# Performance work log

Measured on AMD Instinct MI355X. Metric: run time of the kernel, lower is better.

Reference implementation:

```python
import jax, jax.numpy as jnp
import numpy as np

# Farras first-stage analysis filters [tree][lp/hp][10 taps] (Selesnick fs_farras)
_FARRAS_AF = np.array([
    [[0.0, -0.08838834764832, 0.08838834764832, 0.69587998903400, 0.69587998903400, 0.08838834764832, -0.08838834764832, 0.01122679215254, 0.01122679215254, 0.0],
     [0.0, -0.01122679215254, 0.01122679215254, 0.08838834764832, 0.08838834764832, -0.69587998903400, 0.69587998903400, -0.08838834764832, -0.08838834764832, 0.0]],
    [[0.01122679215254, 0.01122679215254, -0.08838834764832, 0.08838834764832, 0.69587998903400, 0.69587998903400, 0.08838834764832, -0.08838834764832, 0.0, 0.0],
     [0.0, 0.0, -0.08838834764832, -0.08838834764832, 0.69587998903400, -0.69587998903400, 0.08838834764832, 0.08838834764832, 0.01122679215254, -0.01122679215254]]
], dtype=np.float32)

# Kingsbury Q-shift analysis filters (Selesnick dualfilt1)
_DUAL_AF = np.array([
    [[0.03516384, 0.0, -0.08832942, 0.23389032, 0.76027237, 0.58751830, 0.0, -0.11430184, 0.0, 0.0],
     [0.0, 0.0, -0.11430184, 0.0, 0.58751830, -0.76027237, 0.23389032, 0.08832942, 0.0, -0.03516384]],
    [[0.0, 0.0, -0.11430184, 0.0, 0.58751830, 0.76027237, 0.23389032, -0.08832942, 0.0, 0.03516384],
     [-0.03516384, 0.0, 0.08832942, 0.23389032, -0.76027237, 0.58751830, 0.0, -0.11430184, 0.0, 0.0]]
], dtype=np.float32)

# synthesis filters = time-reversed analysis filters
_FSF = np.ascontiguousarray(_FARRAS_AF[:, :, ::-1])
_SF = np.ascontiguousarray(_DUAL_AF[:, :, ::-1])
_INV_SQRT2 = np.float32(1.0 / np.sqrt(2.0))


def _upconv(x, f, axis):
    """Upsample-by-2 then full convolution with taps f along axis (1=H, 2=W), depthwise."""
    L = len(f)
    C = x.shape[-1]
    k = jnp.asarray(np.asarray(f)[::-1].copy(), x.dtype)  # flip taps: true convolution
    if axis == 1:
        kernel = jnp.broadcast_to(k.reshape(L, 1, 1, 1), (L, 1, 1, C))
        dil, pad = (2, 1), ((L - 1, L - 1), (0, 0))
    else:
        kernel = jnp.broadcast_to(k.reshape(1, L, 1, 1), (1, L, 1, C))
        dil, pad = (1, 2), ((0, 0), (L - 1, L - 1))
    return jax.lax.conv_general_dilated(
        x, kernel, window_strides=(1, 1), padding=pad, lhs_dilation=dil,
        dimension_numbers=('NHWC', 'HWIO', 'NHWC'), feature_group_count=C)


def _sfb1d(lo, hi, lp, hp, axis):
    """1D synthesis filter bank (Selesnick sfb1D): upfirdn by 2, periodize, circular shift."""
    L = len(lp)
    N = 2 * lo.shape[axis]
    y = _upconv(lo, lp, axis) + _upconv(hi, hp, axis)  # length N + L - 2 along axis
    head = jax.lax.slice_in_dim(y, 0, L - 2, axis=axis) + jax.lax.slice_in_dim(y, N, N + L - 2, axis=axis)
    body = jax.lax.slice_in_dim(y, L - 2, N, axis=axis)
    return jnp.roll(jnp.concatenate([head, body], axis=axis), 1 - L // 2, axis=axis)


def _sfb2d(lo, hi, sf_row, sf_col):
    """2D separable synthesis: columns first (hi[0]=LH, hi[1]=HL, hi[2]=HH), then rows."""
    lo = _sfb1d(lo, hi[0], sf_col[0], sf_col[1], axis=2)
    h = _sfb1d(hi[1], hi[2], sf_col[0], sf_col[1], axis=2)
    return _sfb1d(lo, h, sf_row[0], sf_row[1], axis=1)


def _add_sub(a, b):
    return (a + b) * _INV_SQRT2, (a - b) * _INV_SQRT2


def _mix(w):
    # w: [2, 2, 3, B, H, W, C]; pair (0,0)<->(1,1) and (0,1)<->(1,0) per orientation
    a00, a11 = _add_sub(w[0, 0], w[1, 1])
    a01, a10 = _add_sub(w[0, 1], w[1, 0])
    return [[a00, a01], [a10, a11]]


def setup_inputs() -> dict:
    key = jax.random.key(0)
    k1, k2, k3 = jax.random.split(key, 3)
    B, C, H2, H4 = 4, 16, 256, 128
    w1 = jax.random.normal(k1, (2, 2, 3, B, H2, H2, C), dtype=jnp.float32)
    w2 = jax.random.normal(k2, (2, 2, 3, B, H4, H4, C), dtype=jnp.float32)
    lo = jax.random.normal(k3, (2, 2, B, H4, H4, C), dtype=jnp.float32)
    return {"w1": w1, "w2": w2, "lo": lo}


def reference(w1, w2, lo):
    wi1, wi2 = _mix(w1), _mix(w2)
    y = None
    for m in range(2):
        for n in range(2):
            x = lo[m, n]                                   # [B, 128, 128, C]
            x = _sfb2d(x, wi2[m][n], _SF[m], _SF[n])       # q-shift stage -> [B, 256, 256, C]
            x = _sfb2d(x, wi1[m][n], _FSF[m], _FSF[n])     # Farras first stage -> [B, 512, 512, C]
            y = x if y is None else y + x
    return y * 0.5
```

## Files before the change

kernel.cpp:

```cpp
#include <hip/hip_runtime.h>

#define INV_SQRT2f 0.70710678118654752440f

__constant__ float c_FAR[2][2][10] = {
  {{0.0f, -0.08838834764832f, 0.08838834764832f, 0.69587998903400f, 0.69587998903400f,
    0.08838834764832f, -0.08838834764832f, 0.01122679215254f, 0.01122679215254f, 0.0f},
   {0.0f, -0.01122679215254f, 0.01122679215254f, 0.08838834764832f, 0.08838834764832f,
    -0.69587998903400f, 0.69587998903400f, -0.08838834764832f, -0.08838834764832f, 0.0f}},
  {{0.01122679215254f, 0.01122679215254f, -0.08838834764832f, 0.08838834764832f, 0.69587998903400f,
    0.69587998903400f, 0.08838834764832f, -0.08838834764832f, 0.0f, 0.0f},
   {0.0f, 0.0f, -0.08838834764832f, -0.08838834764832f, 0.69587998903400f,
    -0.69587998903400f, 0.08838834764832f, 0.08838834764832f, 0.01122679215254f, -0.01122679215254f}}
};
__constant__ float c_DUAL[2][2][10] = {
  {{0.03516384f, 0.0f, -0.08832942f, 0.23389032f, 0.76027237f,
    0.58751830f, 0.0f, -0.11430184f, 0.0f, 0.0f},
   {0.0f, 0.0f, -0.11430184f, 0.0f, 0.58751830f,
    -0.76027237f, 0.23389032f, 0.08832942f, 0.0f, -0.03516384f}},
  {{0.0f, 0.0f, -0.11430184f, 0.0f, 0.58751830f,
    0.76027237f, 0.23389032f, -0.08832942f, 0.0f, 0.03516384f},
   {-0.03516384f, 0.0f, 0.08832942f, 0.23389032f, -0.76027237f,
    0.58751830f, 0.0f, -0.11430184f, 0.0f, 0.0f}}
};

template<int NSZ>
__device__ __forceinline__ void stage_copy(const float* __restrict__ src, float* __restrict__ dst,
                                           int ih0, int iw0, int tid) {
  #pragma unroll
  for (int it = 0; it < 3; ++it) {
    int e = tid + (it << 8);
    if (it < 2 || e < 576) {
      int r = e / 48;
      int cc = e - r * 48;
      int gr = (ih0 + r - 2) & (NSZ - 1);
      int gc = (iw0 + (cc >> 2) - 2) & (NSZ - 1);
      float4 v = *reinterpret_cast<const float4*>(src + (((size_t)gr * NSZ + gc) << 4) + ((cc & 3) << 2));
      *reinterpret_cast<float4*>(dst + (e << 2)) = v;
    }
  }
}

template<int NSZ>
__device__ __forceinline__ void stage_mix(const float* __restrict__ A, const float* __restrict__ B,
                                          float sgn, float* __restrict__ dst,
                                          int ih0, int iw0, int tid) {
  #pragma unroll
  for (int it = 0; it < 3; ++it) {
    int e = tid + (it << 8);
    if (it < 2 || e < 576) {
      int r = e / 48;
      int cc = e - r * 48;
      int gr = (ih0 + r - 2) & (NSZ - 1);
      int gc = (iw0 + (cc >> 2) - 2) & (NSZ - 1);
      size_t off = (((size_t)gr * NSZ + gc) << 4) + ((cc & 3) << 2);
      float4 a = *reinterpret_cast<const float4*>(A + off);
      float4 b = *reinterpret_cast<const float4*>(B + off);
      float4 v;
      v.x = (a.x + sgn * b.x) * INV_SQRT2f;
      v.y = (a.y + sgn * b.y) * INV_SQRT2f;
      v.z = (a.z + sgn * b.z) * INV_SQRT2f;
      v.w = (a.w + sgn * b.w) * INV_SQRT2f;
      *reinterpret_cast<float4*>(dst + (e << 2)) = v;
    }
  }
}

__global__ __launch_bounds__(256) void qshift_kernel(
    const float* __restrict__ w2, const float* __restrict__ loT, float* __restrict__ mid)
{
  __shared__ __align__(16) float sIn[4][12][12][16];

  const int tid = threadIdx.x;
  const int c = tid & 15;
  const int s = tid >> 4;
  const int tw = blockIdx.x;
  const int th = blockIdx.y;
  const int b  = blockIdx.z & 3;
  const int q  = blockIdx.z >> 2;
  const int m = q >> 1, n = q & 1;
  const int j1 = m ^ n;
  const float sgn = m ? -1.0f : 1.0f;
  const int ih0 = th * 8, iw0 = tw * 8;
  const size_t plane = (size_t)128 * 128 * 16;

  stage_copy<128>(loT + ((size_t)(m * 2 + n) * 4 + b) * plane, &sIn[0][0][0][0], ih0, iw0, tid);
  stage_mix<128>(w2 + ((size_t)((0 * 2 + j1) * 3 + 0) * 4 + b) * plane,
                 w2 + ((size_t)((1 * 2 + (1 ^ j1)) * 3 + 0) * 4 + b) * plane,
                 sgn, &sIn[1][0][0][0], ih0, iw0, tid);
  stage_mix<128>(w2 + ((size_t)((0 * 2 + j1) * 3 + 1) * 4 + b) * plane,
                 w2 + ((size_t)((1 * 2 + (1 ^ j1)) * 3 + 1) * 4 + b) * plane,
                 sgn, &sIn[2][0][0][0], ih0, iw0, tid);
  stage_mix<128>(w2 + ((size_t)((0 * 2 + j1) * 3 + 2) * 4 + b) * plane,
                 w2 + ((size_t)((1 * 2 + (1 ^ j1)) * 3 + 2) * 4 + b) * plane,
                 sgn, &sIn[3][0][0][0], ih0, iw0, tid);
  __syncthreads();

  const int pw = s & 1, qw = s >> 1;
  float flp[5], fhp[5];
  #pragma unroll
  for (int j = 0; j < 5; ++j) {
    flp[j] = c_DUAL[n][0][9 - (2 * j + pw)];
    fhp[j] = c_DUAL[n][1][9 - (2 * j + pw)];
  }
  float lo2[12], h2[12];
  #pragma unroll
  for (int r = 0; r < 12; ++r) {
    float lo_v = 0.f, h_v = 0.f;
    #pragma unroll
    for (int j = 0; j < 5; ++j) {
      int x = qw + 4 - j;
      lo_v += flp[j] * sIn[0][r][x][c] + fhp[j] * sIn[1][r][x][c];
      h_v  += flp[j] * sIn[2][r][x][c] + fhp[j] * sIn[3][r][x][c];
    }
    lo2[r] = lo_v;
    h2[r] = h_v;
  }

  float* outQ = mid + ((size_t)q * 4 + b) * (size_t)(256 * 256 * 16);
  #pragma unroll
  for (int nh = 0; nh < 16; ++nh) {
    int ph = nh & 1, qh = nh >> 1;
    float v = 0.f;
    #pragma unroll
    for (int j = 0; j < 5; ++j) {
      v += c_DUAL[m][0][9 - (2 * j + ph)] * lo2[qh + 4 - j]
         + c_DUAL[m][1][9 - (2 * j + ph)] * h2[qh + 4 - j];
    }
    outQ[(((size_t)(ih0 * 2 + nh)) * 256 + (size_t)(iw0 * 2 + s)) * 16 + c] = v;
  }
}

#define CS_RSTRIDE 264

__global__ __launch_bounds__(256) void farras_kernel(
    const float* __restrict__ w1, const float* __restrict__ mid, float* __restrict__ out)
{
  __shared__ __align__(16) float colsum[2 * 12 * CS_RSTRIDE];

  const int tid = threadIdx.x;
  const int c = tid & 15;
  const int s = tid >> 4;
  const int tw = blockIdx.x;
  const int th = blockIdx.y;
  const int b  = blockIdx.z;
  const int ih0 = th * 8, iw0 = tw * 8;
  const size_t plane = (size_t)256 * 256 * 16;

  int role, rr;
  const int c2 = tid & 7;
  if (tid < 64)       { role = 0; rr = tid >> 3; }
  else if (tid < 128) { role = 1; rr = (tid & 63) >> 3; }
  else if (tid < 160) { role = 0; rr = 8 + ((tid & 31) >> 3); }
  else                { role = 1; rr = 8 + ((tid & 31) >> 3); }
  const bool p1act = tid < 192;
  const int gr = (ih0 + rr - 2) & 255;
  const int rowoff = (gr << 12) + 2 * c2;

  int gco[12];
  #pragma unroll
  for (int x = 0; x < 12; ++x) gco[x] = ((iw0 + x - 2) & 255) << 4;

  float acc[16];
  #pragma unroll
  for (int i = 0; i < 16; ++i) acc[i] = 0.f;

  #pragma unroll 1
  for (int q = 0; q < 4; ++q) {
    const int m = q >> 1, n = q & 1;
    const int j1 = m ^ n;
    const float sgn = m ? -1.0f : 1.0f;

    if (p1act) {
      float2 S[16];
      #pragma unroll
      for (int i = 0; i < 16; ++i) S[i] = make_float2(0.f, 0.f);
      const float* tl = &c_FAR[n][0][0];
      const float* tp = &c_FAR[n][1][0];

      if (role == 0) {
        {
          const float* pm = mid + ((size_t)q * 4 + b) * plane + rowoff;
          float2 v[12];
          #pragma unroll
          for (int x = 0; x < 12; ++x) v[x] = *reinterpret_cast<const float2*>(pm + gco[x]);
          #pragma unroll
          for (int x = 0; x < 12; ++x) {
            #pragma unroll
            for (int d = 0; d < 5; ++d) {
              const int qw = x - d;
              if (qw >= 0 && qw <= 7) {
                S[2 * qw].x     += tl[1 + 2 * d] * v[x].x;
                S[2 * qw].y     += tl[1 + 2 * d] * v[x].y;
                S[2 * qw + 1].x += tl[2 * d]     * v[x].x;
                S[2 * qw + 1].y += tl[2 * d]     * v[x].y;
              }
            }
          }
        }
        {
          const float* pa = w1 + ((size_t)((0 * 2 + j1) * 3 + 0) * 4 + b) * plane + rowoff;
          const float* pb = w1 + ((size_t)((1 * 2 + (1 ^ j1)) * 3 + 0) * 4 + b) * plane + rowoff;
          float2 av[12], bv[12];
          #pragma unroll
          for (int x = 0; x < 12; ++x) {
            av[x] = *reinterpret_cast<const float2*>(pa + gco[x]);
            bv[x] = *reinterpret_cast<const float2*>(pb + gco[x]);
          }
          #pragma unroll
          for (int x = 0; x < 12; ++x) {
            float2 mv;
            mv.x = (av[x].x + sgn * bv[x].x) * INV_SQRT2f;
            mv.y = (av[x].y + sgn * bv[x].y) * INV_SQRT2f;
            #pragma unroll
            for (int d = 0; d < 5; ++d) {
              const int qw = x - d;
              if (qw >= 0 && qw <= 7) {
                S[2 * qw].x     += tp[1 + 2 * d] * mv.x;
                S[2 * qw].y     += tp[1 + 2 * d] * mv.y;
                S[2 * qw + 1].x += tp[2 * d]     * mv.x;
                S[2 * qw + 1].y += tp[2 * d]     * mv.y;
              }
            }
          }
        }
      } else {
        {
          const float* pa = w1 + ((size_t)((0 * 2 + j1) * 3 + 1) * 4 + b) * plane + rowoff;
          const float* pb = w1 + ((size_t)((1 * 2 + (1 ^ j1)) * 3 + 1) * 4 + b) * plane + rowoff;
          float2 av[12], bv[12];
          #pragma unroll
          for (int x = 0; x < 12; ++x) {
            av[x] = *reinterpret_cast<const float2*>(pa + gco[x]);
            bv[x] = *reinterpret_cast<const float2*>(pb + gco[x]);
          }
          #pragma unroll
          for (int x = 0; x < 12; ++x) {
            float2 mv;
            mv.x = (av[x].x + sgn * bv[x].x) * INV_SQRT2f;
            mv.y = (av[x].y + sgn * bv[x].y) * INV_SQRT2f;
            #pragma unroll
            for (int d = 0; d < 5; ++d) {
              const int qw = x - d;
              if (qw >= 0 && qw <= 7) {
                S[2 * qw].x     += tl[1 + 2 * d] * mv.x;
                S[2 * qw].y     += tl[1 + 2 * d] * mv.y;
                S[2 * qw + 1].x += tl[2 * d]     * mv.x;
                S[2 * qw + 1].y += tl[2 * d]     * mv.y;
              }
            }
          }
        }
        {
          const float* pa = w1 + ((size_t)((0 * 2 + j1) * 3 + 2) * 4 + b) * plane + rowoff;
          const float* pb = w1 + ((size_t)((1 * 2 + (1 ^ j1)) * 3 + 2) * 4 + b) * plane + rowoff;
          float2 av[12], bv[12];
          #pragma unroll
          for (int x = 0; x < 12; ++x) {
            av[x] = *reinterpret_cast<const float2*>(pa + gco[x]);
            bv[x] = *reinterpret_cast<const float2*>(pb + gco[x]);
          }
          #pragma unroll
          for (int x = 0; x < 12; ++x) {
            float2 mv;
            mv.x = (av[x].x + sgn * bv[x].x) * INV_SQRT2f;
            mv.y = (av[x].y + sgn * bv[x].y) * INV_SQRT2f;
            #pragma unroll
            for (int d = 0; d < 5; ++d) {
              const int qw = x - d;
              if (qw >= 0 && qw <= 7) {
                S[2 * qw].x     += tp[1 + 2 * d] * mv.x;
                S[2 * qw].y     += tp[1 + 2 * d] * mv.y;
                S[2 * qw + 1].x += tp[2 * d]     * mv.x;
                S[2 * qw + 1].y += tp[2 * d]     * mv.y;
              }
            }
          }
        }
      }
      float* dst = &colsum[(role * 12 + rr) * CS_RSTRIDE + 2 * c2];
      #pragma unroll
      for (int nw = 0; nw < 16; ++nw)
        *reinterpret_cast<float2*>(dst + nw * 16) = S[nw];
    }
    __syncthreads();

    {
      float lo2[12], h2[12];
      #pragma unroll
      for (int r = 0; r < 12; ++r) {
        lo2[r] = colsum[(0 * 12 + r) * CS_RSTRIDE + s * 16 + c];
        h2[r]  = colsum[(1 * 12 + r) * CS_RSTRIDE + s * 16 + c];
      }
      #pragma unroll
      for (int nh = 0; nh < 16; ++nh) {
        const int ph = nh & 1, qh = nh >> 1;
        float v = 0.f;
        #pragma unroll
        for (int j = 0; j < 5; ++j) {
          v += c_FAR[m][0][9 - (2 * j + ph)] * lo2[qh + 4 - j]
             + c_FAR[m][1][9 - (2 * j + ph)] * h2[qh + 4 - j];
        }
        acc[nh] += v;
      }
    }
    __syncthreads();
  }

  #pragma unroll
  for (int nh = 0; nh < 16; ++nh) {
    size_t gh = (size_t)(ih0 * 2 + nh);
    size_t gw = (size_t)(iw0 * 2 + s);
    out[(((size_t)b * 512 + gh) * 512 + gw) * 16 + c] = acc[nh] * 0.5f;
  }
}

extern "C" void kernel_launch(void* const* d_in, const int* in_sizes, int n_in,
                              void* d_out, int out_size, void* d_ws, size_t ws_size,
                              hipStream_t stream) {
  const float* w1 = (const float*)d_in[0];
  const float* w2 = (const float*)d_in[1];
  const float* lo = (const float*)d_in[2];
  float* out = (float*)d_out;
  float* mid = (float*)d_ws;

  qshift_kernel<<<dim3(16, 16, 16), 256, 0, stream>>>(w2, lo, mid);
  farras_kernel<<<dim3(32, 32, 4), 256, 0, stream>>>(w1, mid, out);
}
```

Measured before the change: 174.5 us.

## Restructure qshift kernel to compute width filtering in registers from global loads

The qshift kernel no longer stages the raw input tile into shared memory. Each of 192 threads now loads one row of two channels directly from global memory, applies the horizontal upsample-and-filter in registers, and writes only the column-filtered result to a padded shared buffer. This mirrors the farras kernel's existing structure and is meant to cut redundant shared-memory reads and multiply-adds in the width pass. The cost is higher register pressure, 64 threads idle during loading, and float2 instead of float4 global loads.

```diff
diff --git a/kernel.cpp b/kernel.cpp
--- a/kernel.cpp
+++ b/kernel.cpp
@@ -23,52 +23,12 @@
     0.58751830f, 0.0f, -0.11430184f, 0.0f, 0.0f}}
 };
 
-template<int NSZ>
-__device__ __forceinline__ void stage_copy(const float* __restrict__ src, float* __restrict__ dst,
-                                           int ih0, int iw0, int tid) {
-  #pragma unroll
-  for (int it = 0; it < 3; ++it) {
-    int e = tid + (it << 8);
-    if (it < 2 || e < 576) {
-      int r = e / 48;
-      int cc = e - r * 48;
-      int gr = (ih0 + r - 2) & (NSZ - 1);
-      int gc = (iw0 + (cc >> 2) - 2) & (NSZ - 1);
-      float4 v = *reinterpret_cast<const float4*>(src + (((size_t)gr * NSZ + gc) << 4) + ((cc & 3) << 2));
-      *reinterpret_cast<float4*>(dst + (e << 2)) = v;
-    }
-  }
-}
-
-template<int NSZ>
-__device__ __forceinline__ void stage_mix(const float* __restrict__ A, const float* __restrict__ B,
-                                          float sgn, float* __restrict__ dst,
-                                          int ih0, int iw0, int tid) {
-  #pragma unroll
-  for (int it = 0; it < 3; ++it) {
-    int e = tid + (it << 8);
-    if (it < 2 || e < 576) {
-      int r = e / 48;
-      int cc = e - r * 48;
-      int gr = (ih0 + r - 2) & (NSZ - 1);
-      int gc = (iw0 + (cc >> 2) - 2) & (NSZ - 1);
-      size_t off = (((size_t)gr * NSZ + gc) << 4) + ((cc & 3) << 2);
-      float4 a = *reinterpret_cast<const float4*>(A + off);
-      float4 b = *reinterpret_cast<const float4*>(B + off);
-      float4 v;
-      v.x = (a.x + sgn * b.x) * INV_SQRT2f;
-      v.y = (a.y + sgn * b.y) * INV_SQRT2f;
-      v.z = (a.z + sgn * b.z) * INV_SQRT2f;
-      v.w = (a.w + sgn * b.w) * INV_SQRT2f;
-      *reinterpret_cast<float4*>(dst + (e << 2)) = v;
-    }
-  }
-}
+#define CS_RSTRIDE 264
 
 __global__ __launch_bounds__(256) void qshift_kernel(
     const float* __restrict__ w2, const float* __restrict__ loT, float* __restrict__ mid)
 {
-  __shared__ __align__(16) float sIn[4][12][12][16];
+  __shared__ __align__(16) float colsum[2 * 12 * CS_RSTRIDE];
 
   const int tid = threadIdx.x;
   const int c = tid & 15;
@@ -83,43 +43,144 @@
   const int ih0 = th * 8, iw0 = tw * 8;
   const size_t plane = (size_t)128 * 128 * 16;
 
-  stage_copy<128>(loT + ((size_t)(m * 2 + n) * 4 + b) * plane, &sIn[0][0][0][0], ih0, iw0, tid);
-  stage_mix<128>(w2 + ((size_t)((0 * 2 + j1) * 3 + 0) * 4 + b) * plane,
-                 w2 + ((size_t)((1 * 2 + (1 ^ j1)) * 3 + 0) * 4 + b) * plane,
-                 sgn, &sIn[1][0][0][0], ih0, iw0, tid);
-  stage_mix<128>(w2 + ((size_t)((0 * 2 + j1) * 3 + 1) * 4 + b) * plane,
-                 w2 + ((size_t)((1 * 2 + (1 ^ j1)) * 3 + 1) * 4 + b) * plane,
-                 sgn, &sIn[2][0][0][0], ih0, iw0, tid);
-  stage_mix<128>(w2 + ((size_t)((0 * 2 + j1) * 3 + 2) * 4 + b) * plane,
-                 w2 + ((size_t)((1 * 2 + (1 ^ j1)) * 3 + 2) * 4 + b) * plane,
-                 sgn, &sIn[3][0][0][0], ih0, iw0, tid);
+  int role, rr;
+  const int c2 = tid & 7;
+  if (tid < 64)       { role = 0; rr = tid >> 3; }
+  else if (tid < 128) { role = 1; rr = (tid & 63) >> 3; }
+  else if (tid < 160) { role = 0; rr = 8 + ((tid & 31) >> 3); }
+  else                { role = 1; rr = 8 + ((tid & 31) >> 3); }
+  const bool p1act = tid < 192;
+  const int gr = (ih0 + rr - 2) & 127;
+  const int rowoff = (gr << 11) + 2 * c2;
+
+  int gco[12];
+  #pragma unroll
+  for (int x = 0; x < 12; ++x) gco[x] = ((iw0 + x - 2) & 127) << 4;
+
+  if (p1act) {
+    float2 S[16];
+    #pragma unroll
+    for (int i = 0; i < 16; ++i) S[i] = make_float2(0.f, 0.f);
+    const float* tl = &c_DUAL[n][0][0];
+    const float* tp = &c_DUAL[n][1][0];
+
+    if (role == 0) {
+      {
+        const float* pm = loT + ((size_t)(m * 2 + n) * 4 + b) * plane + rowoff;
+        float2 v[12];
+        #pragma unroll
+        for (int x = 0; x < 12; ++x) v[x] = *reinterpret_cast<const float2*>(pm + gco[x]);
+        #pragma unroll
+        for (int x = 0; x < 12; ++x) {
+          #pragma unroll
+          for (int d = 0; d < 5; ++d) {
+            const int qw = x - d;
+            if (qw >= 0 && qw <= 7) {
+              S[2 * qw].x     += tl[1 + 2 * d] * v[x].x;
+              S[2 * qw].y     += tl[1 + 2 * d] * v[x].y;
+              S[2 * qw + 1].x += tl[2 * d]     * v[x].x;
+              S[2 * qw + 1].y += tl[2 * d]     * v[x].y;
+            }
+          }
+        }
+      }
+      {
+        const float* pa = w2 + ((size_t)((0 * 2 + j1) * 3 + 0) * 4 + b) * plane + rowoff;
+        const float* pb = w2 + ((size_t)((1 * 2 + (1 ^ j1)) * 3 + 0) * 4 + b) * plane + rowoff;
+        float2 av[12], bv[12];
+        #pragma unroll
+        for (int x = 0; x < 12; ++x) {
+          av[x] = *reinterpret_cast<const float2*>(pa + gco[x]);
+          bv[x] = *reinterpret_cast<const float2*>(pb + gco[x]);
+        }
+        #pragma unroll
+        for (int x = 0; x < 12; ++x) {
+          float2 mv;
+          mv.x = (av[x].x + sgn * bv[x].x) * INV_SQRT2f;
+          mv.y = (av[x].y + sgn * bv[x].y) * INV_SQRT2f;
+          #pragma unroll
+          for (int d = 0; d < 5; ++d) {
+            const int qw = x - d;
+            if (qw >= 0 && qw <= 7) {
+              S[2 * qw].x     += tp[1 + 2 * d] * mv.x;
+              S[2 * qw].y     += tp[1 + 2 * d] * mv.y;
+              S[2 * qw + 1].x += tp[2 * d]     * mv.x;
+              S[2 * qw + 1].y += tp[2 * d]     * mv.y;
+            }
+          }
+        }
+      }
+    } else {
+      {
+        const float* pa = w2 + ((size_t)((0 * 2 + j1) * 3 + 1) * 4 + b) * plane + rowoff;
+        const float* pb = w2 + ((size_t)((1 * 2 + (1 ^ j1)) * 3 + 1) * 4 + b) * plane + rowoff;
+        float2 av[12], bv[12];
+        #pragma unroll
+        for (int x = 0; x < 12; ++x) {
+          av[x] = *reinterpret_cast<const float2*>(pa + gco[x]);
+          bv[x] = *reinterpret_cast<const float2*>(pb + gco[x]);
+        }
+        #pragma unroll
+        for (int x = 0; x < 12; ++x) {
+          float2 mv;
+          mv.x = (av[x].x + sgn * bv[x].x) * INV_SQRT2f;
+          mv.y = (av[x].y + sgn * bv[x].y) * INV_SQRT2f;
+          #pragma unroll
+          for (int d = 0; d < 5; ++d) {
+            const int qw = x - d;
+            if (qw >= 0 && qw <= 7) {
+              S[2 * qw].x     += tl[1 + 2 * d] * mv.x;
+              S[2 * qw].y     += tl[1 + 2 * d] * mv.y;
+              S[2 * qw + 1].x += tl[2 * d]     * mv.x;
+              S[2 * qw + 1].y += tl[2 * d]     * mv.y;
+            }
+          }
+        }
+      }
+      {
+        const float* pa = w2 + ((size_t)((0 * 2 + j1) * 3 + 2) * 4 + b) * plane + rowoff;
+        const float* pb = w2 + ((size_t)((1 * 2 + (1 ^ j1)) * 3 + 2) * 4 + b) * plane + rowoff;
+        float2 av[12], bv[12];
+        #pragma unroll
+        for (int x = 0; x < 12; ++x) {
+          av[x] = *reinterpret_cast<const float2*>(pa + gco[x]);
+          bv[x] = *reinterpret_cast<const float2*>(pb + gco[x]);
+        }
+        #pragma unroll
+        for (int x = 0; x < 12; ++x) {
+          float2 mv;
+          mv.x = (av[x].x + sgn * bv[x].x) * INV_SQRT2f;
+          mv.y = (av[x].y + sgn * bv[x].y) * INV_SQRT2f;
+          #pragma unroll
+          for (int d = 0; d < 5; ++d) {
+            const int qw = x - d;
+            if (qw >= 0 && qw <= 7) {
+              S[2 * qw].x     += tp[1 + 2 * d] * mv.x;
+              S[2 * qw].y     += tp[1 + 2 * d] * mv.y;
+              S[2 * qw + 1].x += tp[2 * d]     * mv.x;
+              S[2 * qw + 1].y += tp[2 * d]     * mv.y;
+            }
+          }
+        }
+      }
+    }
+    float* dst = &colsum[(role * 12 + rr) * CS_RSTRIDE + 2 * c2];
+    #pragma unroll
+    for (int nw = 0; nw < 16; ++nw)
+      *reinterpret_cast<float2*>(dst + nw * 16) = S[nw];
+  }
   __syncthreads();
 
-  const int pw = s & 1, qw = s >> 1;
-  float flp[5], fhp[5];
-  #pragma unroll
-  for (int j = 0; j < 5; ++j) {
-    flp[j] = c_DUAL[n][0][9 - (2 * j + pw)];
-    fhp[j] = c_DUAL[n][1][9 - (2 * j + pw)];
-  }
   float lo2[12], h2[12];
   #pragma unroll
   for (int r = 0; r < 12; ++r) {
-    float lo_v = 0.f, h_v = 0.f;
-    #pragma unroll
-    for (int j = 0; j < 5; ++j) {
-      int x = qw + 4 - j;
-      lo_v += flp[j] * sIn[0][r][x][c] + fhp[j] * sIn[1][r][x][c];
-      h_v  += flp[j] * sIn[2][r][x][c] + fhp[j] * sIn[3][r][x][c];
-    }
-    lo2[r] = lo_v;
-    h2[r] = h_v;
-  }
-
+    lo2[r] = colsum[(0 * 12 + r) * CS_RSTRIDE + s * 16 + c];
+    h2[r]  = colsum[(1 * 12 + r) * CS_RSTRIDE + s * 16 + c];
+  }
   float* outQ = mid + ((size_t)q * 4 + b) * (size_t)(256 * 256 * 16);
   #pragma unroll
   for (int nh = 0; nh < 16; ++nh) {
-    int ph = nh & 1, qh = nh >> 1;
+    const int ph = nh & 1, qh = nh >> 1;
     float v = 0.f;
     #pragma unroll
     for (int j = 0; j < 5; ++j) {
@@ -129,8 +190,6 @@
     outQ[(((size_t)(ih0 * 2 + nh)) * 256 + (size_t)(iw0 * 2 + s)) * 16 + c] = v;
   }
 }
-
-#define CS_RSTRIDE 264
 
 __global__ __launch_bounds__(256) void farras_kernel(
     const float* __restrict__ w1, const float* __restrict__ mid, float* __restrict__ out)
```

After: 161.7 us. 1.08x faster.
